# Kernel tuning notes

Measured on AMD Instinct MI355X. Metric: run time of the kernel, lower is better.

## Reference

```python
import jax, jax.numpy as jnp
import numpy as np

N_NODES = 50000
N_EDGES = 800000
D = 64
E_DIM = 2
C = 8


def _spline_basis(pseudo, K):
    """Open B-spline basis, degree=1. pseudo: [Ne, E] in [0,1).
    Returns basis B [Ne, S] and flat weight index WI [Ne, S], S = 2**E."""
    E = pseudo.shape[1]
    v = pseudo * (K - 1)
    lo_f = jnp.floor(v)
    frac = v - lo_f
    lo = lo_f.astype(jnp.int32)
    idx = jnp.stack([jnp.clip(lo, 0, K - 1), jnp.clip(lo + 1, 0, K - 1)], axis=-1)  # [Ne,E,2]
    bas = jnp.stack([1.0 - frac, frac], axis=-1)                                   # [Ne,E,2]
    combos = jnp.asarray(
        np.stack(np.meshgrid(*([np.arange(2)] * E), indexing='ij'), -1).reshape(-1, E)
    )  # [S,E]
    d_idx = jnp.arange(E)[None, :]          # broadcast to [S,E]
    B = jnp.prod(bas[:, d_idx, combos], axis=-1)  # [Ne,S]
    stride = (K ** jnp.arange(E)).astype(jnp.int32)  # [E]
    WI = jnp.sum(idx[:, d_idx, combos] * stride[None, None, :], axis=-1)  # [Ne,S]
    return B, WI


def _spline_conv(x, src, dst, pseudo, W, root, bias, K, num_nodes):
    """SplineConv (degree=1, open spline, aggr='mean', root_weight, bias).
    x: [N,Din], W: [K**E, Din, Dout], root: [Din, Dout]."""
    B, WI = _spline_basis(pseudo, K)                 # [Ne,S], [Ne,S]
    Y = jnp.einsum('nd,kdo->nko', x, W)              # [N, K**E, Dout]
    gathered = Y[src[:, None], WI]                   # [Ne, S, Dout]
    m = jnp.einsum('es,eso->eo', B, gathered)        # [Ne, Dout]
    msum = jax.ops.segment_sum(m, dst, num_segments=num_nodes)
    cnt = jax.ops.segment_sum(jnp.ones((m.shape[0], 1), m.dtype), dst, num_segments=num_nodes)
    aggr = msum / jnp.maximum(cnt, 1.0)
    return aggr + x @ root + bias


def setup_inputs() -> dict:
    key = jax.random.key(0)
    ks = jax.random.split(key, 16)
    s = 1.0 / np.sqrt(D)
    return {
        'x': jax.random.normal(ks[0], (N_NODES, D), jnp.float32),
        'edge_index': jax.random.randint(ks[1], (2, N_EDGES), 0, N_NODES, jnp.int32),
        'edge_attr': jax.random.uniform(ks[2], (N_EDGES, E_DIM), jnp.float32),
        'W1': jax.random.normal(ks[3], (3 ** E_DIM, D, D), jnp.float32) * s,
        'root1': jax.random.normal(ks[4], (D, D), jnp.float32) * s,
        'b1': jax.random.normal(ks[5], (D,), jnp.float32) * 0.01,
        'W2': jax.random.normal(ks[6], (5 ** E_DIM, D, D), jnp.float32) * s,
        'root2': jax.random.normal(ks[7], (D, D), jnp.float32) * s,
        'b2': jax.random.normal(ks[8], (D,), jnp.float32) * 0.01,
        'mlp1_w': jax.random.normal(ks[9], (D, D), jnp.float32) * s,
        'mlp1_b': jax.random.normal(ks[10], (D,), jnp.float32) * 0.01,
        'mlp2_w': jax.random.normal(ks[11], (D, C), jnp.float32) * s,
        'mlp2_b': jax.random.normal(ks[12], (C,), jnp.float32) * 0.01,
    }


def reference(x, edge_index, edge_attr, W1, root1, b1, W2, root2, b2,
              mlp1_w, mlp1_b, mlp2_w, mlp2_b):
    N = x.shape[0]
    src, dst = edge_index[0], edge_index[1]
    h = jax.nn.elu(_spline_conv(x, src, dst, edge_attr, W1, root1, b1, 3, N))
    # dropout is identity in eval mode
    h = jax.nn.elu(_spline_conv(h, src, dst, edge_attr, W2, root2, b2, 5, N))
    # task='node', G=0 -> no pooling / no concat
    h = jax.nn.relu(h @ mlp1_w + mlp1_b)
    h = jax.nn.relu(h @ mlp2_w + mlp2_b)
    return h
```

## Files before the change

### kernel.cpp

```cpp
#include <hip/hip_runtime.h>
#include <hip/hip_bf16.h>

typedef __attribute__((ext_vector_type(8))) short short8;
typedef __attribute__((ext_vector_type(4))) short short4v;
typedef __attribute__((ext_vector_type(4))) unsigned int uint4v;
typedef __attribute__((ext_vector_type(4))) float floatx4;
typedef __attribute__((ext_vector_type(16))) float floatx16;

__device__ __forceinline__ unsigned short f2bf(float x) {
  __hip_bfloat16 h = __float2bfloat16(x);
  return __builtin_bit_cast(unsigned short, h);
}
__device__ __forceinline__ float bf2f(unsigned short u) {
  return __builtin_bit_cast(float, (unsigned int)u << 16);
}
__device__ __forceinline__ unsigned int pk_bf16(float lo, float hi) {
  return ((unsigned int)f2bf(hi) << 16) | (unsigned int)f2bf(lo);
}

__device__ __forceinline__ void pack_b_dev(
    const float* __restrict__ W, const float* __restrict__ root,
    unsigned short* __restrict__ Bpk, int K2, int i) {
  int j = i & 7;
  int lane = (i >> 3) & 63;
  int rest = i >> 9;
  int wv = rest & 3, kc = rest >> 2;
  int o = wv * 16 + (lane & 15);
  int p = kc * 32 + ((lane >> 4) & 3) * 8 + j;
  int k = p >> 6, q6 = p & 63;
  float v = (k < K2) ? W[(k << 12) + (q6 << 6) + o] : root[(q6 << 6) + o];
  Bpk[i] = f2bf(v);
}

__global__ __launch_bounds__(256) void prep_kernel(
    const float* __restrict__ W1, const float* __restrict__ root1,
    unsigned short* __restrict__ Bpk1,
    const float* __restrict__ W2, const float* __restrict__ root2,
    unsigned short* __restrict__ Bpk2,
    const float* __restrict__ m1w, unsigned short* __restrict__ m1pk,
    const float4* __restrict__ X, unsigned short* __restrict__ Xbf,
    int* __restrict__ deg, int N) {
  int nbZ = (N + 255) >> 8;
  int b = blockIdx.x, t = threadIdx.x;
  if (b < nbZ) {
    int i = b * 256 + t;
    if (i < N) deg[i] = 0;
    return;
  }
  b -= nbZ;
  if (b < 160) {
    pack_b_dev(W1, root1, Bpk1, 9, b * 256 + t);
    return;
  }
  b -= 160;
  if (b < 416) {
    pack_b_dev(W2, root2, Bpk2, 25, b * 256 + t);
    return;
  }
  b -= 416;
  if (b < 16) {
    pack_b_dev(m1w, m1w, m1pk, 0, b * 256 + t);
    return;
  }
  b -= 16;
  {
    int i = b * 256 + t;
    if (i < N * 16) {
      float4 v = X[i];
      short4v o = {(short)f2bf(v.x), (short)f2bf(v.y),
                   (short)f2bf(v.z), (short)f2bf(v.w)};
      *(short4v*)&Xbf[i * 4] = o;
    }
  }
}

__global__ __launch_bounds__(256) void hist_kernel(
    const int* __restrict__ dst, int* __restrict__ deg, int nE) {
  int e = blockIdx.x * 256 + threadIdx.x;
  if (e < nE) atomicAdd(&deg[dst[e]], 1);
}

__global__ __launch_bounds__(256) void blocksum_kernel(
    const int* __restrict__ deg, int* __restrict__ partial, int N) {
  __shared__ int s[256];
  int t = threadIdx.x, i = blockIdx.x * 256 + t;
  s[t] = (i < N) ? deg[i] : 0;
  __syncthreads();
  for (int off = 128; off > 0; off >>= 1) {
    if (t < off) s[t] += s[t + off];
    __syncthreads();
  }
  if (t == 0) partial[blockIdx.x] = s[0];
}

__global__ __launch_bounds__(256) void blockscan_kernel(
    const int* __restrict__ deg, const int* __restrict__ partial,
    int* __restrict__ row_start, int* __restrict__ cursor,
    int N, int nE, int nb) {
  __shared__ int sp[256];
  __shared__ int s[256];
  __shared__ int base;
  int t = threadIdx.x, i = blockIdx.x * 256 + t;
  int pv = (t < nb) ? partial[t] : 0;
  sp[t] = pv;
  __syncthreads();
  for (int off = 1; off < 256; off <<= 1) {
    int x = (t >= off) ? sp[t - off] : 0;
    __syncthreads();
    sp[t] += x;
    __syncthreads();
  }
  if (t == blockIdx.x) base = sp[t] - pv;
  __syncthreads();
  int v = (i < N) ? deg[i] : 0;
  s[t] = v;
  __syncthreads();
  for (int off = 1; off < 256; off <<= 1) {
    int x = (t >= off) ? s[t - off] : 0;
    __syncthreads();
    s[t] += x;
    __syncthreads();
  }
  if (i < N) {
    int excl = s[t] - v + base;
    row_start[i] = excl;
    cursor[i] = excl;
  }
  if (i == 0) row_start[N] = nE;
}

__global__ __launch_bounds__(256) void scatter_rec_kernel(
    const int* __restrict__ dst, const int* __restrict__ src,
    const float* __restrict__ attr, int* __restrict__ cursor,
    float4* __restrict__ recS, int nE) {
  int e = blockIdx.x * 256 + threadIdx.x;
  if (e < 32) recS[nE + e] = make_float4(0.f, 0.f, 0.f, 0.f);
  if (e >= nE) return;
  int pos = atomicAdd(&cursor[dst[e]], 1);
  float2 a = *(const float2*)&attr[2 * e];
  recS[pos] = make_float4(a.x * 4.f, a.y * 4.f,
                          __builtin_bit_cast(float, src[e] * 64), 0.f);
}

template <int K, int K2, int OUTBF, int NODES, int GRP, int MINW, int PF>
__global__ __launch_bounds__(256, MINW) void spline_layer_kernel(
    const float4* __restrict__ rec, const int* __restrict__ row_start,
    const unsigned short* __restrict__ Xbf, const unsigned short* __restrict__ Bpk,
    const float* __restrict__ bias, void* __restrict__ outv, int N, float uscale) {
  constexpr int RZ = K2 * 64;
  constexpr int AS = RZ + 8;
  constexpr int NKZ = RZ / 32;
  constexpr int NKC = (K2 + 1) * 2;
  __shared__ unsigned short As[NODES * AS];
  __shared__ __align__(16) float invs[16];
  __shared__ int wcur;
  const int t = threadIdx.x, w = t >> 6, lane = t & 63;
  const int nodeBase = blockIdx.x * NODES;

  const int col = lane & 31, half = lane >> 5, col2 = col * 2;
  const float mi0f = (col < K2) ? (float)(col % K) : -1e9f;
  const float mi1f = (col < K2) ? (float)(col / K) : 0.f;

  if (t == 0) wcur = 0;
  if constexpr (NODES < 16) {
    if (w == 3 && lane >= 60) invs[lane - 48] = 1.0f;
  }
  __syncthreads();

  int row;
  if (lane == 0) row = atomicAdd(&wcur, 1);
  row = __shfl(row, 0);
  while (row < NODES) {
    const int node = nodeBase + row;
    if (node < N) {
      floatx16 d0, d1;
#pragma unroll
      for (int i = 0; i < 16; ++i) { d0[i] = 0.f; d1[i] = 0.f; }

      const int beg = row_start[node], end = row_start[node + 1];
      if (lane == 0) invs[row] = 1.f / (float)max(end - beg, 1);

      float4 rjn[8];
      if constexpr (PF) {
        const int ib0 = beg + half * 8;
#pragma unroll
        for (int j = 0; j < 8; ++j) rjn[j] = rec[ib0 + j];
      }
      for (int c0 = beg; c0 < end; c0 += 16) {
        float4 rj[8];
        if constexpr (PF) {
#pragma unroll
          for (int j = 0; j < 8; ++j) rj[j] = rjn[j];
        } else {
          const int ib = c0 + half * 8;
#pragma unroll
          for (int j = 0; j < 8; ++j) rj[j] = rec[ib + j];
        }
        unsigned int xv[8];
#pragma unroll
        for (int j = 0; j < 8; ++j)
          xv[j] = *(const unsigned int*)(Xbf +
                    (__builtin_bit_cast(int, rj[j].z) + col2));
        if constexpr (PF) {
          const int ibn = c0 + 16 + half * 8;
#pragma unroll
          for (int j = 0; j < 8; ++j) rjn[j] = rec[ibn + j];
        }
        short8 A;
        const bool fullc = (end - c0 >= 16);
        const int rem = end - (c0 + half * 8);
#pragma unroll
        for (int j = 0; j < 8; ++j) {
          float t0 = fmaf(rj[j].x, -uscale, mi0f);
          float t1 = fmaf(rj[j].y, -uscale, mi1f);
          float su = fmaxf(0.f, 1.f - fabsf(t0));
          float sv = fmaxf(0.f, 1.f - fabsf(t1));
          float p = su * sv;
          if (!fullc) p = (j < rem) ? p : 0.f;
          A[j] = (short)f2bf(p);
        }
        uint4v blo, bhi;
#pragma unroll
        for (int i = 0; i < 4; ++i) {
          blo[i] = __builtin_amdgcn_perm(xv[2 * i + 1], xv[2 * i], 0x05040100u);
          bhi[i] = __builtin_amdgcn_perm(xv[2 * i + 1], xv[2 * i], 0x07060302u);
        }
        d0 = __builtin_amdgcn_mfma_f32_32x32x16_bf16(
                 A, __builtin_bit_cast(short8, blo), d0, 0, 0, 0);
        d1 = __builtin_amdgcn_mfma_f32_32x32x16_bf16(
                 A, __builtin_bit_cast(short8, bhi), d1, 0, 0, 0);
      }

#pragma unroll
      for (int reg = 0; reg < 16; ++reg) {
        int r = (reg & 3) + 8 * (reg >> 2) + 4 * half;
        if (r < K2)
          *(unsigned int*)&As[row * AS + r * 64 + col2] =
              pk_bf16(d0[reg], d1[reg]);
      }
    } else {
      if (lane == 0) invs[row] = 1.0f;
      for (int i = lane; i < RZ / 2; i += 64)
        ((unsigned int*)&As[row * AS])[i] = 0;
    }
    if (lane == 0) row = atomicAdd(&wcur, 1);
    row = __shfl(row, 0);
  }
  __syncthreads();

  const int mrow = lane & 15, q = lane >> 4;
  const int arow = (NODES < 16) ? min(mrow, NODES - 1) : mrow;
  const int anode = min(nodeBase + arow, N - 1);
  floatx4 aZ0 = {0.f, 0.f, 0.f, 0.f};
  floatx4 aZ1 = {0.f, 0.f, 0.f, 0.f};
  floatx4 aR  = {0.f, 0.f, 0.f, 0.f};
#pragma unroll
  for (int kc0 = 0; kc0 < NKC; kc0 += GRP) {
    short8 av[GRP], bv[GRP];
#pragma unroll
    for (int u = 0; u < GRP; ++u) {
      const int kc = kc0 + u;
      if (kc < NKZ)
        av[u] = *(const short8*)&As[arow * AS + kc * 32 + q * 8];
      else
        av[u] = *(const short8*)&Xbf[(size_t)anode * 64 + (kc - NKZ) * 32 + q * 8];
      bv[u] = *(const short8*)&Bpk[(((size_t)kc * 4 + w) * 64 + lane) * 8];
    }
#pragma unroll
    for (int u = 0; u < GRP; ++u) {
      const int kc = kc0 + u;
      if (kc >= NKZ)
        aR = __builtin_amdgcn_mfma_f32_16x16x32_bf16(av[u], bv[u], aR, 0, 0, 0);
      else if ((kc0 / GRP) & 1)
        aZ1 = __builtin_amdgcn_mfma_f32_16x16x32_bf16(av[u], bv[u], aZ1, 0, 0, 0);
      else
        aZ0 = __builtin_amdgcn_mfma_f32_16x16x32_bf16(av[u], bv[u], aZ0, 0, 0, 0);
    }
  }

  const int o = w * 16 + mrow;
  const float bvs = bias[o];
  const floatx4 invv = *(const floatx4*)&invs[q * 4];
#pragma unroll
  for (int reg = 0; reg < 4; ++reg) {
    int rloc = q * 4 + reg;
    int node = nodeBase + rloc;
    if (rloc < NODES && node < N) {
      float v = (aZ0[reg] + aZ1[reg]) * invv[reg] + aR[reg] + bvs;
      v = v > 0.f ? v : (expf(v) - 1.f);
      if (OUTBF)
        ((unsigned short*)outv)[(size_t)node * 64 + o] = f2bf(v);
      else
        ((float*)outv)[(size_t)node * 64 + o] = v;
    }
  }
}

__global__ __launch_bounds__(256) void head_kernel(
    const unsigned short* __restrict__ h2bf, const unsigned short* __restrict__ m1pk,
    const float* __restrict__ m1b, const float* __restrict__ m2w,
    const float* __restrict__ m2b, float* __restrict__ out, int N) {
  __shared__ unsigned short Hs[64 * 72];
  __shared__ unsigned short Ts[64 * 72];
  __shared__ float W2s[512];
  const int t = threadIdx.x, w = t >> 6, lane = t & 63;
  const int n0 = blockIdx.x * 64;

  for (int i = t; i < 512; i += 256) {
    int row = i >> 3, cg = i & 7;
    int n = n0 + row;
    floatx4 val = {0.f, 0.f, 0.f, 0.f};
    if (n < N) val = *(const floatx4*)&h2bf[(size_t)n * 64 + cg * 8];
    *(floatx4*)&Hs[row * 72 + cg * 8] = val;
  }
  for (int i = t; i < 512; i += 256) W2s[i] = m2w[i];
  __syncthreads();

  const int mrow = lane & 15, q = lane >> 4;
  const int o = w * 16 + mrow;
  const float bv = m1b[o];
#pragma unroll
  for (int rg = 0; rg < 4; ++rg) {
    floatx4 acc = {0.f, 0.f, 0.f, 0.f};
#pragma unroll
    for (int kc = 0; kc < 2; ++kc) {
      short8 a = *(const short8*)&Hs[(rg * 16 + mrow) * 72 + kc * 32 + q * 8];
      short8 b = *(const short8*)&m1pk[(((size_t)kc * 4 + w) * 64 + lane) * 8];
      acc = __builtin_amdgcn_mfma_f32_16x16x32_bf16(a, b, acc, 0, 0, 0);
    }
#pragma unroll
    for (int reg = 0; reg < 4; ++reg) {
      int row = rg * 16 + q * 4 + reg;
      float v = acc[reg] + bv;
      Ts[row * 72 + o] = f2bf(v > 0.f ? v : 0.f);
    }
  }
  __syncthreads();

  for (int i = t; i < 512; i += 256) {
    int nl = i >> 3, c = i & 7;
    int n = n0 + nl;
    if (n >= N) continue;
    float s = m2b[c];
    for (int d = 0; d < 64; ++d) s += bf2f(Ts[nl * 72 + d]) * W2s[d * 8 + c];
    out[(size_t)n * 8 + c] = s > 0.f ? s : 0.f;
  }
}

extern "C" void kernel_launch(void* const* d_in, const int* in_sizes, int n_in,
                              void* d_out, int out_size, void* d_ws, size_t ws_size,
                              hipStream_t stream) {
  const float* x     = (const float*)d_in[0];
  const int*   ei    = (const int*)d_in[1];
  const float* attr  = (const float*)d_in[2];
  const float* W1    = (const float*)d_in[3];
  const float* root1 = (const float*)d_in[4];
  const float* b1    = (const float*)d_in[5];
  const float* W2    = (const float*)d_in[6];
  const float* root2 = (const float*)d_in[7];
  const float* b2    = (const float*)d_in[8];
  const float* m1w   = (const float*)d_in[9];
  const float* m1b   = (const float*)d_in[10];
  const float* m2w   = (const float*)d_in[11];
  const float* m2b   = (const float*)d_in[12];

  const int N  = in_sizes[0] / 64;
  const int nE = in_sizes[1] / 2;
  const int* src  = ei;
  const int* dstv = ei + nE;
  float* out = (float*)d_out;

  int* deg       = (int*)d_ws;
  int* row_start = deg + N;
  int* cursor    = row_start + (N + 1);
  int* partial   = cursor + N;
  char* pbase = (char*)(partial + 256);
  pbase = (char*)(((uintptr_t)pbase + 15) & ~(uintptr_t)15);
  float4* recS = (float4*)pbase;
  unsigned short* Xbf  = (unsigned short*)(recS + nE + 32);
  unsigned short* h1bf = Xbf + (size_t)N * 64;
  unsigned short* h2bf = h1bf + (size_t)N * 64;
  unsigned short* Bpk1 = h2bf + (size_t)N * 64;
  unsigned short* Bpk2 = Bpk1 + 64 * 640;
  unsigned short* m1pk = Bpk2 + 64 * 1664;

  dim3 blk(256);
  int nbN  = (N + 255) / 256;
  int nbE  = (nE + 255) / 256;
  int nbF  = (N + 15) / 16;
  int nbH  = (N + 63) / 64;
  int nbP  = nbN + 160 + 416 + 16 + (N * 16 + 255) / 256;

  prep_kernel<<<nbP, blk, 0, stream>>>(W1, root1, Bpk1, W2, root2, Bpk2,
                                       m1w, m1pk, (const float4*)x, Xbf,
                                       deg, N);

  hist_kernel<<<nbE, blk, 0, stream>>>(dstv, deg, nE);
  blocksum_kernel<<<nbN, blk, 0, stream>>>(deg, partial, N);
  blockscan_kernel<<<nbN, blk, 0, stream>>>(deg, partial, row_start, cursor,
                                            N, nE, nbN);
  scatter_rec_kernel<<<nbE, blk, 0, stream>>>(dstv, src, attr, cursor, recS, nE);

  spline_layer_kernel<3, 9, 1, 16, 4, 4, 0><<<nbF, blk, 0, stream>>>(
      recS, row_start, Xbf, Bpk1, b1, h1bf, N, 0.5f);

  spline_layer_kernel<5, 25, 1, 16, 4, 4, 1><<<nbF, blk, 0, stream>>>(
      recS, row_start, h1bf, Bpk2, b2, h2bf, N, 1.0f);

  head_kernel<<<nbH, blk, 0, stream>>>(h2bf, m1pk, m1b, m2w, m2b, out, N);
}
```

Measured before the change: 303.0 us.

## Software-pipeline edge gather and basis compute one chunk ahead; shrink layer-2 node tile

The edge loop in the spline layer now prefetches two chunks of edge records ahead and issues the feature gathers and basis computation for the next chunk before the current chunk's MFMAs. The goal is to hide gather latency behind matrix work in both layers. The layer-2 node tile drops from 16 to 12 nodes per block, which shrinks its shared-memory footprint to allow more resident blocks, and the zero padding after the records grows to 48 entries to cover the deeper prefetch. This raises register pressure, which could lower occupancy.

```diff
diff --git a/kernel.cpp b/kernel.cpp
--- a/kernel.cpp
+++ b/kernel.cpp
@@ -134,7 +134,7 @@
     const float* __restrict__ attr, int* __restrict__ cursor,
     float4* __restrict__ recS, int nE) {
   int e = blockIdx.x * 256 + threadIdx.x;
-  if (e < 32) recS[nE + e] = make_float4(0.f, 0.f, 0.f, 0.f);
+  if (e < 48) recS[nE + e] = make_float4(0.f, 0.f, 0.f, 0.f);
   if (e >= nE) return;
   int pos = atomicAdd(&cursor[dst[e]], 1);
   float2 a = *(const float2*)&attr[2 * e];
@@ -142,7 +142,7 @@
                           __builtin_bit_cast(float, src[e] * 64), 0.f);
 }
 
-template <int K, int K2, int OUTBF, int NODES, int GRP, int MINW, int PF>
+template <int K, int K2, int OUTBF, int NODES, int GRP, int MINW>
 __global__ __launch_bounds__(256, MINW) void spline_layer_kernel(
     const float4* __restrict__ rec, const int* __restrict__ row_start,
     const unsigned short* __restrict__ Xbf, const unsigned short* __restrict__ Bpk,
@@ -180,45 +180,46 @@
       const int beg = row_start[node], end = row_start[node + 1];
       if (lane == 0) invs[row] = 1.f / (float)max(end - beg, 1);
 
-      float4 rjn[8];
-      if constexpr (PF) {
-        const int ib0 = beg + half * 8;
-#pragma unroll
-        for (int j = 0; j < 8; ++j) rjn[j] = rec[ib0 + j];
-      }
-      for (int c0 = beg; c0 < end; c0 += 16) {
-        float4 rj[8];
-        if constexpr (PF) {
-#pragma unroll
-          for (int j = 0; j < 8; ++j) rj[j] = rjn[j];
-        } else {
-          const int ib = c0 + half * 8;
-#pragma unroll
-          for (int j = 0; j < 8; ++j) rj[j] = rec[ib + j];
-        }
-        unsigned int xv[8];
-#pragma unroll
-        for (int j = 0; j < 8; ++j)
-          xv[j] = *(const unsigned int*)(Xbf +
-                    (__builtin_bit_cast(int, rj[j].z) + col2));
-        if constexpr (PF) {
-          const int ibn = c0 + 16 + half * 8;
-#pragma unroll
-          for (int j = 0; j < 8; ++j) rjn[j] = rec[ibn + j];
-        }
-        short8 A;
-        const bool fullc = (end - c0 >= 16);
-        const int rem = end - (c0 + half * 8);
+      auto basis = [&](const float4* rr, int cc0) -> short8 {
+        short8 Ao;
+        const bool fullc = (end - cc0 >= 16);
+        const int rem = end - (cc0 + half * 8);
 #pragma unroll
         for (int j = 0; j < 8; ++j) {
-          float t0 = fmaf(rj[j].x, -uscale, mi0f);
-          float t1 = fmaf(rj[j].y, -uscale, mi1f);
+          float t0 = fmaf(rr[j].x, -uscale, mi0f);
+          float t1 = fmaf(rr[j].y, -uscale, mi1f);
           float su = fmaxf(0.f, 1.f - fabsf(t0));
           float sv = fmaxf(0.f, 1.f - fabsf(t1));
           float p = su * sv;
           if (!fullc) p = (j < rem) ? p : 0.f;
-          A[j] = (short)f2bf(p);
+          Ao[j] = (short)f2bf(p);
         }
+        return Ao;
+      };
+
+      const int ibh = beg + half * 8;
+      float4 rjn[8];
+      unsigned int xv[8], xvn[8];
+      short8 A, An;
+
+#pragma unroll
+      for (int j = 0; j < 8; ++j) rjn[j] = rec[ibh + j];
+#pragma unroll
+      for (int j = 0; j < 8; ++j)
+        xv[j] = *(const unsigned int*)(Xbf +
+                  (__builtin_bit_cast(int, rjn[j].z) + col2));
+      A = basis(rjn, beg);
+#pragma unroll
+      for (int j = 0; j < 8; ++j) rjn[j] = rec[ibh + 16 + j];
+
+      for (int c0 = beg; c0 < end; c0 += 16) {
+#pragma unroll
+        for (int j = 0; j < 8; ++j)
+          xvn[j] = *(const unsigned int*)(Xbf +
+                     (__builtin_bit_cast(int, rjn[j].z) + col2));
+        An = basis(rjn, c0 + 16);
+#pragma unroll
+        for (int j = 0; j < 8; ++j) rjn[j] = rec[c0 + 32 + half * 8 + j];
         uint4v blo, bhi;
 #pragma unroll
         for (int i = 0; i < 4; ++i) {
@@ -229,6 +230,9 @@
                  A, __builtin_bit_cast(short8, blo), d0, 0, 0, 0);
         d1 = __builtin_amdgcn_mfma_f32_32x32x16_bf16(
                  A, __builtin_bit_cast(short8, bhi), d1, 0, 0, 0);
+        A = An;
+#pragma unroll
+        for (int j = 0; j < 8; ++j) xv[j] = xvn[j];
       }
 
 #pragma unroll
@@ -377,7 +381,7 @@
   char* pbase = (char*)(partial + 256);
   pbase = (char*)(((uintptr_t)pbase + 15) & ~(uintptr_t)15);
   float4* recS = (float4*)pbase;
-  unsigned short* Xbf  = (unsigned short*)(recS + nE + 32);
+  unsigned short* Xbf  = (unsigned short*)(recS + nE + 48);
   unsigned short* h1bf = Xbf + (size_t)N * 64;
   unsigned short* h2bf = h1bf + (size_t)N * 64;
   unsigned short* Bpk1 = h2bf + (size_t)N * 64;
@@ -387,7 +391,8 @@
   dim3 blk(256);
   int nbN  = (N + 255) / 256;
   int nbE  = (nE + 255) / 256;
-  int nbF  = (N + 15) / 16;
+  int nbF1 = (N + 15) / 16;
+  int nbF2 = (N + 11) / 12;
   int nbH  = (N + 63) / 64;
   int nbP  = nbN + 160 + 416 + 16 + (N * 16 + 255) / 256;
 
@@ -401,10 +406,10 @@
                                             N, nE, nbN);
   scatter_rec_kernel<<<nbE, blk, 0, stream>>>(dstv, src, attr, cursor, recS, nE);
 
-  spline_layer_kernel<3, 9, 1, 16, 4, 4, 0><<<nbF, blk, 0, stream>>>(
+  spline_layer_kernel<3, 9, 1, 16, 4, 4><<<nbF1, blk, 0, stream>>>(
       recS, row_start, Xbf, Bpk1, b1, h1bf, N, 0.5f);
 
-  spline_layer_kernel<5, 25, 1, 16, 4, 4, 1><<<nbF, blk, 0, stream>>>(
+  spline_layer_kernel<5, 25, 1, 12, 4, 4><<<nbF2, blk, 0, stream>>>(
       recS, row_start, h1bf, Bpk2, b2, h2bf, N, 1.0f);
 
   head_kernel<<<nbH, blk, 0, stream>>>(h2bf, m1pk, m1b, m2w, m2b, out, N);
```

Result: slower. 343.8 us (+13.4%).
